# Kernel tuning notes

Hardware: AMD Instinct MI355X
Metric: run time of the kernel (lower is better)

## Reference

```python
import jax, jax.numpy as jnp
import numpy as np

EPS = 1e-6

def _rms_norm(x, w):
    rms = jnp.sqrt(jnp.mean(x * x, axis=-1, keepdims=True) + EPS)
    return x / rms * w

def _rotate_half(x):
    x1, x2 = jnp.split(x, 2, axis=-1)
    return jnp.concatenate([-x2, x1], axis=-1)

def _apply_rope(qk, cos, sin):
    return qk * cos + _rotate_half(qk) * sin

def setup_inputs() -> dict:
    key = jax.random.key(0)
    ks = jax.random.split(key, 4)
    B, N, C, H = 4, 2048, 1024, 16
    hd = C // H
    x = jax.random.normal(ks[0], (B, N, C), dtype=jnp.float32)
    rope_cos = jax.random.uniform(ks[1], (1, 1, N, hd), dtype=jnp.float32)
    rope_sin = jax.random.uniform(ks[2], (1, 1, N, hd), dtype=jnp.float32)
    w_qkv = jax.random.normal(ks[3], (3 * C, C), dtype=jnp.float32) * (C ** -0.5)
    w_proj = jax.random.normal(jax.random.fold_in(key, 10), (C, C), dtype=jnp.float32) * (C ** -0.5)
    b_proj = jnp.zeros((C,), dtype=jnp.float32)
    q_norm_w = jnp.ones((hd,), dtype=jnp.float32)
    k_norm_w = jnp.ones((hd,), dtype=jnp.float32)
    return {"x": x, "rope_cos": rope_cos, "rope_sin": rope_sin, "w_qkv": w_qkv,
            "w_proj": w_proj, "b_proj": b_proj, "q_norm_w": q_norm_w, "k_norm_w": k_norm_w}

def reference(x, rope_cos, rope_sin, w_qkv, w_proj, b_proj, q_norm_w, k_norm_w):
    B, N, C = x.shape
    H = 16
    hd = C // H
    scale = hd ** -0.5
    qkv = jnp.einsum('bnc,dc->bnd', x, w_qkv)          # [B,N,3C]
    qkv = qkv.reshape(B, N, 3, H, hd).transpose(2, 0, 3, 1, 4)  # [3,B,H,N,hd]
    q, k, v = qkv[0], qkv[1], qkv[2]
    q = _rms_norm(q, q_norm_w)
    k = _rms_norm(k, k_norm_w)
    q = _apply_rope(q, rope_cos, rope_sin)
    k = _apply_rope(k, rope_cos, rope_sin)
    attn = jnp.einsum('bhqd,bhkd->bhqk', q, k) * scale
    attn = jax.nn.softmax(attn, axis=-1)
    out = jnp.einsum('bhqk,bhkd->bhqd', attn, v)        # [B,H,N,hd]
    out = out.transpose(0, 2, 1, 3).reshape(B, N, C)
    return jnp.einsum('bnc,dc->bnd', out, w_proj) + b_proj
```

## Files before the change

kernel.cpp:

```cpp
#include <hip/hip_runtime.h>
#include <stdint.h>
#include <math.h>

typedef unsigned short u16;
typedef __attribute__((ext_vector_type(8))) short short8;
typedef __attribute__((ext_vector_type(4))) float floatx4;
typedef __attribute__((ext_vector_type(4))) unsigned short ushort4v;

#define MFMA16(a, b, c) __builtin_amdgcn_mfma_f32_16x16x32_bf16(a, b, c, 0, 0, 0)

constexpr int B_ = 4, N_ = 2048, C_ = 1024, H_ = 16, HD = 64;
constexpr size_t SZ_X = (size_t)B_ * N_ * C_;
constexpr size_t SZ_WQKV = (size_t)3 * C_ * C_;
constexpr size_t SZ_WPROJ = (size_t)C_ * C_;
constexpr size_t SZ_QKV = (size_t)B_ * H_ * N_ * HD;

#define QSCALE 0.1803368801111204f

__device__ __forceinline__ u16 f2bf(float f) {
  union { float f; uint32_t u; } c; c.f = f;
  uint32_t u = c.u;
  return (u16)((u + 0x7FFFu + ((u >> 16) & 1u)) >> 16);
}
__device__ __forceinline__ u16 f2bf_fast(float f) {
  union { float f; uint32_t u; } c; c.f = f;
  return (u16)((c.u + 0x8000u) >> 16);
}
__device__ __forceinline__ float bf2f(u16 h) {
  union { uint32_t u; float f; } c; c.u = ((uint32_t)h) << 16;
  return c.f;
}
__device__ __forceinline__ void async16(const u16* g, u16* l) {
  __builtin_amdgcn_global_load_lds(
      (const __attribute__((address_space(1))) void*)g,
      (__attribute__((address_space(3))) void*)l, 16, 0, 0);
}

__global__ __launch_bounds__(256) void cvt_bf16(const float* __restrict__ in,
                                                u16* __restrict__ out, int n4) {
  int i = blockIdx.x * 256 + threadIdx.x;
  if (i >= n4) return;
  float4 v = ((const float4*)in)[i];
  ushort4v o;
  o.x = f2bf(v.x); o.y = f2bf(v.y); o.z = f2bf(v.z); o.w = f2bf(v.w);
  ((ushort4v*)out)[i] = o;
}

template <int MODE>
__global__ __launch_bounds__(256) void gemm_bt(
    const u16* __restrict__ A, const u16* __restrict__ Bm, int K,
    u16* __restrict__ qb, u16* __restrict__ kb, u16* __restrict__ vtb,
    float* __restrict__ outf, const float* __restrict__ bias, int N) {
  const int tid = threadIdx.x;
  const int wave = tid >> 6;
  const int lane = tid & 63;
  const int quad = lane >> 4;
  const int l16 = lane & 15;
  const int bm0 = blockIdx.x * 128;
  const int bn0 = blockIdx.y * 128;
  const int wm = (wave >> 1) * 64;
  const int wn = (wave & 1) * 64;

  __shared__ __align__(16) u16 As[128 * 32];
  __shared__ __align__(16) u16 Bs[128 * 32];

  floatx4 acc[4][4];
#pragma unroll
  for (int i = 0; i < 4; ++i)
#pragma unroll
    for (int j = 0; j < 4; ++j)
#pragma unroll
      for (int r = 0; r < 4; ++r) acc[i][j][r] = 0.f;

  for (int k0 = 0; k0 < K; k0 += 32) {
    __syncthreads();
#pragma unroll
    for (int j = 0; j < 2; ++j) {
      const int seg = tid + j * 256;
      const int row = seg >> 2;
      const int ks = (seg & 3) * 8;
      u16* la = As + (size_t)(wave * 64 + j * 256) * 8;
      u16* lb = Bs + (size_t)(wave * 64 + j * 256) * 8;
      async16(A + (size_t)(bm0 + row) * K + k0 + ks, la);
      async16(Bm + (size_t)(bn0 + row) * K + k0 + ks, lb);
    }
    __syncthreads();

    short8 af[4], bf[4];
#pragma unroll
    for (int t = 0; t < 4; ++t)
      af[t] = *(const short8*)(As + (wm + t * 16 + l16) * 32 + quad * 8);
#pragma unroll
    for (int t = 0; t < 4; ++t)
      bf[t] = *(const short8*)(Bs + (wn + t * 16 + l16) * 32 + quad * 8);
#pragma unroll
    for (int i = 0; i < 4; ++i)
#pragma unroll
      for (int j = 0; j < 4; ++j)
        acc[i][j] = MFMA16(af[i], bf[j], acc[i][j]);
  }

  if (MODE == 0) {
#pragma unroll
    for (int i = 0; i < 4; ++i)
#pragma unroll
      for (int j = 0; j < 4; ++j)
#pragma unroll
        for (int r = 0; r < 4; ++r) {
          const int m = bm0 + wm + i * 16 + quad * 4 + r;
          const int n = bn0 + wn + j * 16 + l16;
          const u16 bv = f2bf(acc[i][j][r]);
          const int t = n >> 10;
          const int h = (n >> 6) & 15;
          const int e = n & 63;
          const int b = m >> 11;
          const int tok = m & 2047;
          const size_t bh = (size_t)(b * 16 + h);
          if (t == 0)      qb[(bh * 2048 + tok) * 64 + e] = bv;
          else if (t == 1) kb[(bh * 2048 + tok) * 64 + e] = bv;
          else             vtb[(bh * 64 + e) * 2048 + tok] = bv;
        }
  } else {
#pragma unroll
    for (int i = 0; i < 4; ++i)
#pragma unroll
      for (int j = 0; j < 4; ++j)
#pragma unroll
        for (int r = 0; r < 4; ++r) {
          const int m = bm0 + wm + i * 16 + quad * 4 + r;
          const int n = bn0 + wn + j * 16 + l16;
          outf[(size_t)m * N + n] = acc[i][j][r] + bias[n];
        }
  }
}

__global__ __launch_bounds__(256) void normrope(
    u16* __restrict__ qb, u16* __restrict__ kb,
    const float* __restrict__ cosp, const float* __restrict__ sinp,
    const float* __restrict__ qw, const float* __restrict__ kw) {
  const int lane = threadIdx.x & 63;
  const int gid = blockIdx.x * 4 + (threadIdx.x >> 6);
  const int BHN = B_ * H_ * N_;
  const bool isq = gid < BHN;
  const int rid = isq ? gid : gid - BHN;
  u16* buf = isq ? qb : kb;
  const float* w = isq ? qw : kw;
  const int n = rid & (N_ - 1);
  const size_t base = (size_t)rid * 64;

  float v = bf2f(buf[base + lane]);
  float ss = v * v;
#pragma unroll
  for (int d = 1; d < 64; d <<= 1) ss += __shfl_xor(ss, d);
  const float inv = 1.0f / sqrtf(ss * (1.0f / 64.0f) + 1e-6f);
  const float xn = v * inv * w[lane];
  const float p = __shfl_xor(xn, 32);
  const float rot = (lane < 32) ? -p : p;
  float o = xn * cosp[n * 64 + lane] + rot * sinp[n * 64 + lane];
  if (isq) o *= QSCALE;
  buf[base + lane] = f2bf(o);
}

__global__ __launch_bounds__(256, 4) void attn_kernel(
    const u16* __restrict__ qb, const u16* __restrict__ kb,
    const u16* __restrict__ vtb, u16* __restrict__ ob) {
  const int tid = threadIdx.x;
  const int wave = tid >> 6, lane = tid & 63;
  const int quad = lane >> 4, l16 = lane & 15;
  const int bh = blockIdx.y;
  const int q0 = blockIdx.x * 128;

  __shared__ __align__(16) u16 Ksf[64 * 64];
  __shared__ __align__(16) u16 Vsf[64 * 64];
  __shared__ __align__(16) u16 Ps[4][2][16 * 72];

  const u16* qptr = qb + (size_t)bh * (2048 * 64);
  const u16* kptr = kb + (size_t)bh * (2048 * 64);
  const u16* vptr = vtb + (size_t)bh * (64 * 2048);

  const int s0 = tid, s1 = tid + 256;
  const int ct0 = s0 >> 7, ct1 = s1 >> 7;
  const int hf0 = (s0 >> 6) & 1, hf1 = (s1 >> 6) & 1;
  const u16* kg0 = kptr + (size_t)(ct0 * 16 + l16) * 64 + hf0 * 32 + quad * 8;
  const u16* kg1 = kptr + (size_t)(ct1 * 16 + l16) * 64 + hf1 * 32 + quad * 8;
  const u16* vg0 = vptr + (size_t)(ct0 * 16 + l16) * 2048 + hf0 * 32 + quad * 8;
  const u16* vg1 = vptr + (size_t)(ct1 * 16 + l16) * 2048 + hf1 * 32 + quad * 8;
  u16* kl0 = Ksf + (size_t)(wave * 64) * 8;
  u16* kl1 = Ksf + (size_t)(256 + wave * 64) * 8;
  u16* vl0 = Vsf + (size_t)(wave * 64) * 8;
  u16* vl1 = Vsf + (size_t)(256 + wave * 64) * 8;

  short8 aq[2][2];
#pragma unroll
  for (int sub = 0; sub < 2; ++sub) {
    const int qrow = q0 + wave * 32 + sub * 16 + l16;
#pragma unroll
    for (int hf = 0; hf < 2; ++hf)
      aq[sub][hf] =
          *(const short8*)(qptr + (size_t)qrow * 64 + hf * 32 + quad * 8);
  }

  short8 ones;
#pragma unroll
  for (int j = 0; j < 8; ++j) ones[j] = (short)0x3F80;

  floatx4 o[2][4], ol[2];
#pragma unroll
  for (int sub = 0; sub < 2; ++sub) {
#pragma unroll
    for (int r = 0; r < 4; ++r) ol[sub][r] = 0.f;
#pragma unroll
    for (int et = 0; et < 4; ++et)
#pragma unroll
      for (int r = 0; r < 4; ++r) o[sub][et][r] = 0.f;
  }

  for (int n0 = 0; n0 < 2048; n0 += 64) {
    __syncthreads();
    async16(kg0 + (size_t)n0 * 64, kl0);
    async16(kg1 + (size_t)n0 * 64, kl1);
    async16(vg0 + n0, vl0);
    async16(vg1 + n0, vl1);
    __syncthreads();

    floatx4 sc[2][4];
#pragma unroll
    for (int ct = 0; ct < 4; ++ct) {
      const short8 kb0 = *(const short8*)(Ksf + ct * 1024 + lane * 8);
      const short8 kb1 = *(const short8*)(Ksf + ct * 1024 + 512 + lane * 8);
#pragma unroll
      for (int sub = 0; sub < 2; ++sub) {
        floatx4 z;
#pragma unroll
        for (int r = 0; r < 4; ++r) z[r] = 0.f;
        z = MFMA16(aq[sub][0], kb0, z);
        sc[sub][ct] = MFMA16(aq[sub][1], kb1, z);
      }
    }

#pragma unroll
    for (int sub = 0; sub < 2; ++sub)
#pragma unroll
      for (int ct = 0; ct < 4; ++ct)
#pragma unroll
        for (int r = 0; r < 4; ++r) {
          const float p = exp2f(sc[sub][ct][r]);
          Ps[wave][sub][(quad * 4 + r) * 72 + ct * 16 + l16] = f2bf_fast(p);
        }

    __asm__ volatile("s_waitcnt lgkmcnt(0)" ::: "memory");

    short8 pa[2][2];
#pragma unroll
    for (int sub = 0; sub < 2; ++sub) {
      pa[sub][0] = *(const short8*)(&Ps[wave][sub][l16 * 72 + quad * 8]);
      pa[sub][1] = *(const short8*)(&Ps[wave][sub][l16 * 72 + 32 + quad * 8]);
    }

#pragma unroll
    for (int et = 0; et < 4; ++et) {
      const short8 vb0 = *(const short8*)(Vsf + et * 1024 + lane * 8);
      const short8 vb1 = *(const short8*)(Vsf + et * 1024 + 512 + lane * 8);
#pragma unroll
      for (int sub = 0; sub < 2; ++sub) {
        o[sub][et] = MFMA16(pa[sub][0], vb0, o[sub][et]);
        o[sub][et] = MFMA16(pa[sub][1], vb1, o[sub][et]);
      }
    }
#pragma unroll
    for (int sub = 0; sub < 2; ++sub) {
      ol[sub] = MFMA16(pa[sub][0], ones, ol[sub]);
      ol[sub] = MFMA16(pa[sub][1], ones, ol[sub]);
    }
  }

  const int b = bh >> 4, h = bh & 15;
#pragma unroll
  for (int sub = 0; sub < 2; ++sub) {
    float inv[4];
#pragma unroll
    for (int r = 0; r < 4; ++r) inv[r] = 1.0f / ol[sub][r];
#pragma unroll
    for (int et = 0; et < 4; ++et)
#pragma unroll
      for (int r = 0; r < 4; ++r) {
        const int row = q0 + wave * 32 + sub * 16 + quad * 4 + r;
        const int e = et * 16 + l16;
        ob[((size_t)b * 2048 + row) * 1024 + h * 64 + e] =
            f2bf(o[sub][et][r] * inv[r]);
      }
  }
}

extern "C" void kernel_launch(void* const* d_in, const int* in_sizes, int n_in,
                              void* d_out, int out_size, void* d_ws, size_t ws_size,
                              hipStream_t stream) {
  const float* x     = (const float*)d_in[0];
  const float* cosp  = (const float*)d_in[1];
  const float* sinp  = (const float*)d_in[2];
  const float* wqkv  = (const float*)d_in[3];
  const float* wproj = (const float*)d_in[4];
  const float* bias  = (const float*)d_in[5];
  const float* qw    = (const float*)d_in[6];
  const float* kw    = (const float*)d_in[7];
  float* out = (float*)d_out;

  u16* xb     = (u16*)d_ws;
  u16* wqkvb  = xb + SZ_X;
  u16* wprojb = wqkvb + SZ_WQKV;
  u16* qb     = wprojb + SZ_WPROJ;
  u16* kb     = qb + SZ_QKV;
  u16* vtb    = kb + SZ_QKV;
  u16* ob     = vtb + SZ_QKV;

  cvt_bf16<<<(int)(SZ_X / 4 / 256), 256, 0, stream>>>(x, xb, (int)(SZ_X / 4));
  cvt_bf16<<<(int)(SZ_WQKV / 4 / 256), 256, 0, stream>>>(wqkv, wqkvb, (int)(SZ_WQKV / 4));
  cvt_bf16<<<(int)(SZ_WPROJ / 4 / 256), 256, 0, stream>>>(wproj, wprojb, (int)(SZ_WPROJ / 4));

  gemm_bt<0><<<dim3(64, 24), 256, 0, stream>>>(xb, wqkvb, 1024, qb, kb, vtb,
                                               nullptr, nullptr, 3072);
  normrope<<<(2 * B_ * H_ * N_) / 4, 256, 0, stream>>>(qb, kb, cosp, sinp, qw, kw);
  attn_kernel<<<dim3(16, 64), 256, 0, stream>>>(qb, kb, vtb, ob);
  gemm_bt<1><<<dim3(64, 8), 256, 0, stream>>>(ob, wprojb, 1024, nullptr, nullptr,
                                              nullptr, out, bias, 1024);
}
```

Before: 359.4 us.

## Fuse RMSNorm+RoPE into QKV GEMM epilogue and enlarge attention query tile

Moves the q/k RMS normalisation and rotary embedding into the QKV GEMM epilogue, computed on fp32 accumulators with shuffles across the 16-lane head group. This drops the separate normrope kernel and its extra read/write of q and k. The attention kernel now processes 256 query rows per block (4 subtiles per wave), remaps blocks so heads are grouped per XCD, and computes S^T so the exp results pack directly into LDS. The trade-off is higher register pressure and fewer blocks in the attention grid.

```diff
diff --git a/kernel.cpp b/kernel.cpp
--- a/kernel.cpp
+++ b/kernel.cpp
@@ -25,10 +25,6 @@
 __device__ __forceinline__ u16 f2bf_fast(float f) {
   union { float f; uint32_t u; } c; c.f = f;
   return (u16)((c.u + 0x8000u) >> 16);
-}
-__device__ __forceinline__ float bf2f(u16 h) {
-  union { uint32_t u; float f; } c; c.u = ((uint32_t)h) << 16;
-  return c.f;
 }
 __device__ __forceinline__ void async16(const u16* g, u16* l) {
   __builtin_amdgcn_global_load_lds(
@@ -50,7 +46,9 @@
 __global__ __launch_bounds__(256) void gemm_bt(
     const u16* __restrict__ A, const u16* __restrict__ Bm, int K,
     u16* __restrict__ qb, u16* __restrict__ kb, u16* __restrict__ vtb,
-    float* __restrict__ outf, const float* __restrict__ bias, int N) {
+    float* __restrict__ outf, const float* __restrict__ bias, int N,
+    const float* __restrict__ cosp, const float* __restrict__ sinp,
+    const float* __restrict__ qw, const float* __restrict__ kw) {
   const int tid = threadIdx.x;
   const int wave = tid >> 6;
   const int lane = tid & 63;
@@ -101,25 +99,58 @@
   }
 
   if (MODE == 0) {
-#pragma unroll
-    for (int i = 0; i < 4; ++i)
-#pragma unroll
-      for (int j = 0; j < 4; ++j)
+    const int hb = (bn0 + wn) >> 6;
+    const int t = hb >> 4;
+    const int h = hb & 15;
+    if (t < 2) {
+      const float* w = (t == 0) ? qw : kw;
+      u16* dstb = (t == 0) ? qb : kb;
+      float wv[4];
+#pragma unroll
+      for (int j = 0; j < 4; ++j) wv[j] = w[j * 16 + l16];
+#pragma unroll
+      for (int i = 0; i < 4; ++i)
 #pragma unroll
         for (int r = 0; r < 4; ++r) {
           const int m = bm0 + wm + i * 16 + quad * 4 + r;
-          const int n = bn0 + wn + j * 16 + l16;
-          const u16 bv = f2bf(acc[i][j][r]);
-          const int t = n >> 10;
-          const int h = (n >> 6) & 15;
-          const int e = n & 63;
-          const int b = m >> 11;
-          const int tok = m & 2047;
-          const size_t bh = (size_t)(b * 16 + h);
-          if (t == 0)      qb[(bh * 2048 + tok) * 64 + e] = bv;
-          else if (t == 1) kb[(bh * 2048 + tok) * 64 + e] = bv;
-          else             vtb[(bh * 64 + e) * 2048 + tok] = bv;
+          const int b = m >> 11, tok = m & 2047;
+          float ss = 0.f;
+#pragma unroll
+          for (int j = 0; j < 4; ++j) ss += acc[i][j][r] * acc[i][j][r];
+          ss += __shfl_xor(ss, 1);
+          ss += __shfl_xor(ss, 2);
+          ss += __shfl_xor(ss, 4);
+          ss += __shfl_xor(ss, 8);
+          const float inv = 1.0f / sqrtf(ss * (1.0f / 64.0f) + 1e-6f);
+          float xn[4];
+#pragma unroll
+          for (int j = 0; j < 4; ++j) xn[j] = acc[i][j][r] * inv * wv[j];
+          u16* dst = dstb + ((size_t)(b * 16 + h) * 2048 + tok) * 64;
+#pragma unroll
+          for (int j = 0; j < 4; ++j) {
+            const int e = j * 16 + l16;
+            const float cs = cosp[tok * 64 + e];
+            const float sn = sinp[tok * 64 + e];
+            const float rot = (j < 2) ? -xn[j + 2] : xn[j - 2];
+            float o = xn[j] * cs + rot * sn;
+            if (t == 0) o *= QSCALE;
+            dst[e] = f2bf(o);
+          }
         }
+    } else {
+#pragma unroll
+      for (int i = 0; i < 4; ++i)
+#pragma unroll
+        for (int j = 0; j < 4; ++j)
+#pragma unroll
+          for (int r = 0; r < 4; ++r) {
+            const int m = bm0 + wm + i * 16 + quad * 4 + r;
+            const int b = m >> 11, tok = m & 2047;
+            const int e = j * 16 + l16;
+            vtb[((size_t)(b * 16 + h) * 64 + e) * 2048 + tok] =
+                f2bf(acc[i][j][r]);
+          }
+    }
   } else {
 #pragma unroll
     for (int i = 0; i < 4; ++i)
@@ -134,45 +165,22 @@
   }
 }
 
-__global__ __launch_bounds__(256) void normrope(
-    u16* __restrict__ qb, u16* __restrict__ kb,
-    const float* __restrict__ cosp, const float* __restrict__ sinp,
-    const float* __restrict__ qw, const float* __restrict__ kw) {
-  const int lane = threadIdx.x & 63;
-  const int gid = blockIdx.x * 4 + (threadIdx.x >> 6);
-  const int BHN = B_ * H_ * N_;
-  const bool isq = gid < BHN;
-  const int rid = isq ? gid : gid - BHN;
-  u16* buf = isq ? qb : kb;
-  const float* w = isq ? qw : kw;
-  const int n = rid & (N_ - 1);
-  const size_t base = (size_t)rid * 64;
-
-  float v = bf2f(buf[base + lane]);
-  float ss = v * v;
-#pragma unroll
-  for (int d = 1; d < 64; d <<= 1) ss += __shfl_xor(ss, d);
-  const float inv = 1.0f / sqrtf(ss * (1.0f / 64.0f) + 1e-6f);
-  const float xn = v * inv * w[lane];
-  const float p = __shfl_xor(xn, 32);
-  const float rot = (lane < 32) ? -p : p;
-  float o = xn * cosp[n * 64 + lane] + rot * sinp[n * 64 + lane];
-  if (isq) o *= QSCALE;
-  buf[base + lane] = f2bf(o);
-}
-
-__global__ __launch_bounds__(256, 4) void attn_kernel(
+__global__ __launch_bounds__(256) void attn_kernel(
     const u16* __restrict__ qb, const u16* __restrict__ kb,
     const u16* __restrict__ vtb, u16* __restrict__ ob) {
   const int tid = threadIdx.x;
   const int wave = tid >> 6, lane = tid & 63;
   const int quad = lane >> 4, l16 = lane & 15;
-  const int bh = blockIdx.y;
-  const int q0 = blockIdx.x * 128;
+
+  const int id = blockIdx.x + blockIdx.y * 8;
+  const int xcd = id & 7;
+  const int s = id >> 3;
+  const int bh = xcd + 8 * (s & 7);
+  const int q0 = (s >> 3) * 256;
 
   __shared__ __align__(16) u16 Ksf[64 * 64];
   __shared__ __align__(16) u16 Vsf[64 * 64];
-  __shared__ __align__(16) u16 Ps[4][2][16 * 72];
+  __shared__ __align__(16) u16 Ps[4][4][16 * 72];
 
   const u16* qptr = qb + (size_t)bh * (2048 * 64);
   const u16* kptr = kb + (size_t)bh * (2048 * 64);
@@ -190,10 +198,10 @@
   u16* vl0 = Vsf + (size_t)(wave * 64) * 8;
   u16* vl1 = Vsf + (size_t)(256 + wave * 64) * 8;
 
-  short8 aq[2][2];
-#pragma unroll
-  for (int sub = 0; sub < 2; ++sub) {
-    const int qrow = q0 + wave * 32 + sub * 16 + l16;
+  short8 aq[4][2];
+#pragma unroll
+  for (int sub = 0; sub < 4; ++sub) {
+    const int qrow = q0 + wave * 64 + sub * 16 + l16;
 #pragma unroll
     for (int hf = 0; hf < 2; ++hf)
       aq[sub][hf] =
@@ -204,9 +212,9 @@
 #pragma unroll
   for (int j = 0; j < 8; ++j) ones[j] = (short)0x3F80;
 
-  floatx4 o[2][4], ol[2];
-#pragma unroll
-  for (int sub = 0; sub < 2; ++sub) {
+  floatx4 o[4][4], ol[4];
+#pragma unroll
+  for (int sub = 0; sub < 4; ++sub) {
 #pragma unroll
     for (int r = 0; r < 4; ++r) ol[sub][r] = 0.f;
 #pragma unroll
@@ -223,38 +231,33 @@
     async16(vg1 + n0, vl1);
     __syncthreads();
 
-    floatx4 sc[2][4];
-#pragma unroll
-    for (int ct = 0; ct < 4; ++ct) {
-      const short8 kb0 = *(const short8*)(Ksf + ct * 1024 + lane * 8);
-      const short8 kb1 = *(const short8*)(Ksf + ct * 1024 + 512 + lane * 8);
-#pragma unroll
-      for (int sub = 0; sub < 2; ++sub) {
+#pragma unroll
+    for (int t = 0; t < 4; ++t) {
+      const short8 kf0 = *(const short8*)(Ksf + t * 1024 + lane * 8);
+      const short8 kf1 = *(const short8*)(Ksf + t * 1024 + 512 + lane * 8);
+#pragma unroll
+      for (int sub = 0; sub < 4; ++sub) {
         floatx4 z;
 #pragma unroll
         for (int r = 0; r < 4; ++r) z[r] = 0.f;
-        z = MFMA16(aq[sub][0], kb0, z);
-        sc[sub][ct] = MFMA16(aq[sub][1], kb1, z);
+        z = MFMA16(kf0, aq[sub][0], z);
+        z = MFMA16(kf1, aq[sub][1], z);
+        ushort4v pk;
+        pk.x = f2bf_fast(__builtin_amdgcn_exp2f(z[0]));
+        pk.y = f2bf_fast(__builtin_amdgcn_exp2f(z[1]));
+        pk.z = f2bf_fast(__builtin_amdgcn_exp2f(z[2]));
+        pk.w = f2bf_fast(__builtin_amdgcn_exp2f(z[3]));
+        *(ushort4v*)(Ps[wave][sub] + l16 * 72 + t * 16 + quad * 4) = pk;
       }
     }
 
-#pragma unroll
-    for (int sub = 0; sub < 2; ++sub)
-#pragma unroll
-      for (int ct = 0; ct < 4; ++ct)
-#pragma unroll
-        for (int r = 0; r < 4; ++r) {
-          const float p = exp2f(sc[sub][ct][r]);
-          Ps[wave][sub][(quad * 4 + r) * 72 + ct * 16 + l16] = f2bf_fast(p);
-        }
-
     __asm__ volatile("s_waitcnt lgkmcnt(0)" ::: "memory");
 
-    short8 pa[2][2];
-#pragma unroll
-    for (int sub = 0; sub < 2; ++sub) {
-      pa[sub][0] = *(const short8*)(&Ps[wave][sub][l16 * 72 + quad * 8]);
-      pa[sub][1] = *(const short8*)(&Ps[wave][sub][l16 * 72 + 32 + quad * 8]);
+    short8 pa[4][2];
+#pragma unroll
+    for (int sub = 0; sub < 4; ++sub) {
+      pa[sub][0] = *(const short8*)(Ps[wave][sub] + l16 * 72 + quad * 8);
+      pa[sub][1] = *(const short8*)(Ps[wave][sub] + l16 * 72 + 32 + quad * 8);
     }
 
 #pragma unroll
@@ -262,13 +265,13 @@
       const short8 vb0 = *(const short8*)(Vsf + et * 1024 + lane * 8);
       const short8 vb1 = *(const short8*)(Vsf + et * 1024 + 512 + lane * 8);
 #pragma unroll
-      for (int sub = 0; sub < 2; ++sub) {
+      for (int sub = 0; sub < 4; ++sub) {
         o[sub][et] = MFMA16(pa[sub][0], vb0, o[sub][et]);
         o[sub][et] = MFMA16(pa[sub][1], vb1, o[sub][et]);
       }
     }
 #pragma unroll
-    for (int sub = 0; sub < 2; ++sub) {
+    for (int sub = 0; sub < 4; ++sub) {
       ol[sub] = MFMA16(pa[sub][0], ones, ol[sub]);
       ol[sub] = MFMA16(pa[sub][1], ones, ol[sub]);
     }
@@ -276,7 +279,7 @@
 
   const int b = bh >> 4, h = bh & 15;
 #pragma unroll
-  for (int sub = 0; sub < 2; ++sub) {
+  for (int sub = 0; sub < 4; ++sub) {
     float inv[4];
 #pragma unroll
     for (int r = 0; r < 4; ++r) inv[r] = 1.0f / ol[sub][r];
@@ -284,7 +287,7 @@
     for (int et = 0; et < 4; ++et)
 #pragma unroll
       for (int r = 0; r < 4; ++r) {
-        const int row = q0 + wave * 32 + sub * 16 + quad * 4 + r;
+        const int row = q0 + wave * 64 + sub * 16 + quad * 4 + r;
         const int e = et * 16 + l16;
         ob[((size_t)b * 2048 + row) * 1024 + h * 64 + e] =
             f2bf(o[sub][et][r] * inv[r]);
@@ -318,9 +321,10 @@
   cvt_bf16<<<(int)(SZ_WPROJ / 4 / 256), 256, 0, stream>>>(wproj, wprojb, (int)(SZ_WPROJ / 4));
 
   gemm_bt<0><<<dim3(64, 24), 256, 0, stream>>>(xb, wqkvb, 1024, qb, kb, vtb,
-                                               nullptr, nullptr, 3072);
-  normrope<<<(2 * B_ * H_ * N_) / 4, 256, 0, stream>>>(qb, kb, cosp, sinp, qw, kw);
-  attn_kernel<<<dim3(16, 64), 256, 0, stream>>>(qb, kb, vtb, ob);
+                                               nullptr, nullptr, 3072,
+                                               cosp, sinp, qw, kw);
+  attn_kernel<<<dim3(8, 64), 256, 0, stream>>>(qb, kb, vtb, ob);
   gemm_bt<1><<<dim3(64, 8), 256, 0, stream>>>(ob, wprojb, 1024, nullptr, nullptr,
-                                              nullptr, out, bias, 1024);
-}
+                                              nullptr, out, bias, 1024,
+                                              nullptr, nullptr, nullptr, nullptr);
+}
```

New measurement: 371.7 us. 1.03x slower.
